# Kernel optimization log

Measured on AMD Instinct MI355X. Metric: run time of the kernel, lower is better.

The kernel has to match this reference:

```python
import jax, jax.numpy as jnp
import numpy as np

B, L, V, D = 512, 41, 4, 64        # batch, seq_len=41 (hard-coded in source), vocab=DNA, d_model=64
NL, DI, N, DTR, K = 3, 128, 16, 4, 4  # n_layer, d_inner=2*D, d_state, dt_rank=ceil(D/16), d_conv
NS = 3  # three parallel stacks (layers1/2/3)


def setup_inputs() -> dict:
    key = jax.random.key(0)
    ks = jax.random.split(key, 16)
    s = 0.02
    nrm = lambda k, sh: jax.random.normal(k, sh, jnp.float32) * s
    A_log = jnp.log(jnp.arange(1, N + 1, dtype=jnp.float32))  # S4D-real init
    return {
        "input_ids": jax.random.randint(ks[0], (B, L), 0, V),
        "embedding": nrm(ks[1], (V, D)),
        # per-stack, per-layer Mamba block params, stacked [NS, NL, ...]
        "in_proj": nrm(ks[2], (NS, NL, D, 2 * DI)),
        "conv_w": nrm(ks[3], (NS, NL, DI, 1, K)),
        "conv_b": jnp.zeros((NS, NL, DI), jnp.float32),
        "x_proj": nrm(ks[4], (NS, NL, DI, DTR + 2 * N)),
        "dt_w": nrm(ks[5], (NS, NL, DTR, DI)),
        "dt_b": jnp.full((NS, NL, DI), -2.0, jnp.float32),
        "A_log": jnp.broadcast_to(A_log, (NS, NL, DI, N)) + 0.0,
        "Dp": jnp.ones((NS, NL, DI), jnp.float32),
        "out_proj": nrm(ks[6], (NS, NL, DI, D)),
        "norm_w": jnp.ones((NS, NL, D), jnp.float32),
        "norm_f_w": jnp.ones((D,), jnp.float32),
        "fusion_w": jnp.zeros((NS,), jnp.float32),  # softmax-weighted fusion of the 3 representations
        # LastDense MLP head: 64*41 -> 384 -> 16 -> 1 (dropout is eval-mode identity)
        "W1": nrm(ks[7], (D * L, 384)), "b1": jnp.zeros((384,), jnp.float32),
        "W2": nrm(ks[8], (384, 16)), "b2": jnp.zeros((16,), jnp.float32),
        "W3": nrm(ks[9], (16, 1)), "b3": jnp.zeros((1,), jnp.float32),
    }


def rmsnorm(x, w, eps=1e-5):
    return x * jax.lax.rsqrt(jnp.mean(x * x, axis=-1, keepdims=True) + eps) * w


def silu(x):
    return x * jax.nn.sigmoid(x)


def mamba_block(x, ip, cw, cb, xp, dw, db, al, dp, op):
    # x: [B, L, D]
    bsz = x.shape[0]
    u, res = jnp.split(x @ ip, 2, axis=-1)  # each [B, L, DI]
    # causal depthwise conv1d (torch padding=3 then [..., :L] == left-pad K-1)
    uc = jax.lax.conv_general_dilated(
        u.transpose(0, 2, 1), cw, window_strides=(1,), padding=[(K - 1, 0)],
        feature_group_count=DI, dimension_numbers=("NCH", "OIH", "NCH"))
    u = silu((uc + cb[None, :, None]).transpose(0, 2, 1))  # [B, L, DI]
    dbl = u @ xp  # [B, L, DTR+2N]
    dt = jax.nn.softplus(dbl[..., :DTR] @ dw + db)           # [B, L, DI]
    Bm = dbl[..., DTR:DTR + N]                               # [B, L, N]
    C = dbl[..., DTR + N:]                                   # [B, L, N]
    A = -jnp.exp(al)                                         # [DI, N]
    dA = jnp.exp(dt[..., None] * A)                          # [B, L, DI, N]
    dBu = dt[..., None] * Bm[:, :, None, :] * u[..., None]   # [B, L, DI, N]

    def step(h, xs):
        dA_t, dBu_t, C_t = xs
        h = dA_t * h + dBu_t                                 # [B, DI, N]
        return h, jnp.einsum("bdn,bn->bd", h, C_t)

    h0 = jnp.zeros((bsz, DI, N), x.dtype)
    _, ys = jax.lax.scan(step, h0, (dA.transpose(1, 0, 2, 3), dBu.transpose(1, 0, 2, 3), C.transpose(1, 0, 2)))
    y = ys.transpose(1, 0, 2) + u * dp                       # [B, L, DI]
    return (y * silu(res)) @ op                              # [B, L, D]


def _forward(input_ids, embedding, in_proj, conv_w, conv_b, x_proj, dt_w, dt_b,
             A_log, Dp, out_proj, norm_w, norm_f_w, fusion_w, W1, b1, W2, b2, W3, b3):
    emb = embedding[input_ids]  # [B, L, D]

    def run_stack(ip, cw, cb, xp, dw, db, al, dp, op, nw):
        x = emb
        for i in range(NL):  # residual: x + MambaBlock(RMSNorm(x))
            x = x + mamba_block(rmsnorm(x, nw[i]), ip[i], cw[i], cb[i], xp[i], dw[i], db[i], al[i], dp[i], op[i])
        return x

    stack_out = jax.vmap(run_stack)(in_proj, conv_w, conv_b, x_proj, dt_w, dt_b,
                                    A_log, Dp, out_proj, norm_w)  # [NS, B, L, D]
    stack_out = rmsnorm(stack_out, norm_f_w)  # final norm_f per stack
    fused = jnp.einsum("s,sbld->bld", jax.nn.softmax(fusion_w), stack_out)  # fusion of 3 reps
    flat = fused.reshape(fused.shape[0], L * D)
    h = jax.nn.relu(flat @ W1 + b1)
    h = jax.nn.relu(h @ W2 + b2)
    logits = (h @ W3 + b3)[:, 0]
    return jax.nn.sigmoid(logits)  # [B]


def reference(input_ids, embedding, in_proj, conv_w, conv_b, x_proj, dt_w, dt_b,
              A_log, Dp, out_proj, norm_w, norm_f_w, fusion_w, W1, b1, W2, b2, W3, b3):
    return _forward(input_ids, embedding, in_proj, conv_w, conv_b, x_proj, dt_w, dt_b,
                    A_log, Dp, out_proj, norm_w, norm_f_w, fusion_w, W1, b1, W2, b2, W3, b3)
```

## Files before the change

### kernel.cpp

```cpp
#include <hip/hip_runtime.h>
#include <hip/hip_bf16.h>
#include <math.h>

#define Bq  512
#define Lq  41
#define Vq  4
#define Dq  64
#define NLq 3
#define DIq 128
#define Nq  16
#define DTRq 4
#define Kq  4
#define NSq 3
#define H1q 384
#define H2q 16
#define FLATq (Lq*Dq)

typedef __attribute__((ext_vector_type(8))) short frag8;
typedef __attribute__((ext_vector_type(4))) float f32x4;

__device__ __forceinline__ float b2f(unsigned short u) {
    union { float f; unsigned int i; } v; v.i = ((unsigned int)u) << 16; return v.f;
}
__device__ __forceinline__ unsigned short f2b_rne(float f) {
    union { float f; unsigned int i; } v; v.f = f;
    unsigned int x = v.i;
    return (unsigned short)((x + 0x7fffu + ((x >> 16) & 1u)) >> 16);
}
__device__ __forceinline__ unsigned short f2b_tr(float f) {
    union { float f; unsigned int i; } v; v.f = f;
    return (unsigned short)(v.i >> 16);
}
__device__ __forceinline__ float fast_rcp(float x) { return __builtin_amdgcn_rcpf(x); }

__global__ __launch_bounds__(256) void prep_kernel(const float* __restrict__ W1,
                                                   const float* __restrict__ in_proj,
                                                   const float* __restrict__ x_proj,
                                                   const float* __restrict__ out_proj,
                                                   unsigned short* __restrict__ W1b,
                                                   unsigned short* __restrict__ Wb_in,
                                                   unsigned short* __restrict__ xp_b,
                                                   unsigned short* __restrict__ op_b) {
    const int bx = blockIdx.x;
    if (bx < 246) {
        __shared__ float t[64][65];
        const int k0 = (bx / 6) * 64, n0 = (bx % 6) * 64;
        for (int idx = threadIdx.x; idx < 4096; idx += 256) {
            int kr = idx >> 6, nc = idx & 63;
            t[kr][nc] = W1[(size_t)(k0 + kr) * H1q + n0 + nc];
        }
        __syncthreads();
        for (int idx = threadIdx.x; idx < 4096; idx += 256) {
            int nr = idx >> 6, kc = idx & 63;
            W1b[(size_t)(n0 + nr) * FLATq + k0 + kc] = f2b_rne(t[kc][nr]);
        }
        return;
    }
    int idx = (bx - 246) * 256 + threadIdx.x;
    if (idx < 9*256*64) {
        int sl = idx >> 14, rem = idx & 16383;
        int n = rem >> 6, k = rem & 63;
        Wb_in[idx] = f2b_rne(in_proj[(size_t)sl*16384 + k*256 + n]);
    } else if (idx < 9*256*64 + 9*48*128) {
        int i2 = idx - 9*256*64;
        int sl = i2 / 6144, rem = i2 % 6144;
        int c = rem >> 7, k = rem & 127;
        float v = (c < 36) ? x_proj[(size_t)sl*(128*36) + k*36 + c] : 0.f;
        xp_b[i2] = f2b_rne(v);
    } else if (idx < 9*256*64 + 9*48*128 + 9*64*128) {
        int i3 = idx - (9*256*64 + 9*48*128);
        int sl = i3 >> 13, rem = i3 & 8191;
        int n = rem >> 7, k = rem & 127;
        op_b[i3] = f2b_rne(out_proj[(size_t)sl*8192 + k*64 + n]);
    }
}

__global__ __launch_bounds__(256, 4) void mamba_stack(
    unsigned short* __restrict__ Xn,
    const int* __restrict__ ids,
    const float* __restrict__ emb,
    const unsigned short* __restrict__ Wb_in,
    const float* __restrict__ conv_w,
    const float* __restrict__ conv_b,
    const unsigned short* __restrict__ xp_b,
    const float* __restrict__ dt_w,
    const float* __restrict__ dt_b,
    const float* __restrict__ A_log,
    const float* __restrict__ Dp,
    const unsigned short* __restrict__ op_b,
    const float* __restrict__ norm_w,
    const float* __restrict__ norm_f_w,
    const float* __restrict__ fusion_w)
{
    const int b = blockIdx.x, s = blockIdx.y, tid = threadIdx.x;
    const int wave = tid >> 6, lane = tid & 63;
    const int nl = lane & 15, quad = lane >> 4;

    __shared__ float          xt  [Lq][64];
    __shared__ unsigned short u_lb[48][136];
    __shared__ unsigned short rs_lb[Lq][128];
    __shared__ __align__(16) char un_buf[6912];
    unsigned short (*xn_lb)[72] = (unsigned short(*)[72])un_buf;
    float          (*dbl_s)[40] = (float(*)[40])un_buf;

    for (int l = wave; l < Lq; l += 4) {
        int id = ids[b * Lq + l];
        xt[l][lane] = emb[id * Dq + lane];
    }

    for (int layer = 0; layer < NLq; ++layer) {
        const int sl = s * NLq + layer;

        {
            const float nwv = norm_w[(size_t)sl * Dq + lane];
            for (int l = wave; l < 48; l += 4) {
                if (l < Lq) {
                    float v  = xt[l][lane];
                    float ss = v * v;
                    #pragma unroll
                    for (int off = 32; off; off >>= 1) ss += __shfl_xor(ss, off, 64);
                    float scale = __builtin_amdgcn_rsqf(ss * (1.0f / Dq) + 1e-5f);
                    xn_lb[l][lane] = f2b_tr(v * scale * nwv);
                } else {
                    xn_lb[l][lane] = 0;
                }
            }
        }
        __syncthreads();

        {
            #pragma unroll
            for (int t = 0; t < 12; ++t) {
                const int id = wave * 12 + t;
                const int mt = id >> 4, nt = id & 15;
                const unsigned short* Wp = Wb_in + ((size_t)(sl * 256 + nt * 16 + nl)) * 64 + quad * 8;
                frag8 a0 = *(const frag8*)&xn_lb[mt * 16 + nl][quad * 8];
                frag8 a1 = *(const frag8*)&xn_lb[mt * 16 + nl][32 + quad * 8];
                frag8 b0 = *(const frag8*)&Wp[0];
                frag8 b1 = *(const frag8*)&Wp[32];
                f32x4 c = {0.f, 0.f, 0.f, 0.f};
                c = __builtin_amdgcn_mfma_f32_16x16x32_bf16(a0, b0, c, 0, 0, 0);
                c = __builtin_amdgcn_mfma_f32_16x16x32_bf16(a1, b1, c, 0, 0, 0);
                const int col = nt * 16 + nl;
                const int r0 = mt * 16 + quad * 4;
                if (col < DIq) {
                    #pragma unroll
                    for (int r = 0; r < 4; ++r) u_lb[r0 + r][col] = f2b_tr(c[r]);
                } else {
                    const int d = col - DIq;
                    #pragma unroll
                    for (int r = 0; r < 4; ++r) {
                        int row = r0 + r;
                        if (row < Lq) {
                            float v = c[r];
                            rs_lb[row][d] = f2b_tr(v * fast_rcp(1.f + __expf(-v)));
                        }
                    }
                }
            }
        }
        __syncthreads();

        {
            const float* cw = conv_w + (size_t)sl * (DIq * Kq);
            const int d = tid >> 1, half = tid & 1;
            const float c0 = cw[d*4+0], c1 = cw[d*4+1], c2 = cw[d*4+2], c3 = cw[d*4+3];
            const float cbv = conv_b[(size_t)sl * DIq + d];
            float w0 = 0.f, w1 = 0.f, w2 = 0.f;
            if (half) { w0 = b2f(u_lb[18][d]); w1 = b2f(u_lb[19][d]); w2 = b2f(u_lb[20][d]); }
            const int base = half ? 21 : 0;
            const int cnt  = half ? 20 : 21;
            for (int i = 0; i < cnt; ++i) {
                int l = base + i;
                float cur = b2f(u_lb[l][d]);
                float a = fmaf(w0, c0, fmaf(w1, c1, fmaf(w2, c2, fmaf(cur, c3, cbv))));
                u_lb[l][d] = f2b_tr(a * fast_rcp(1.f + __expf(-a)));
                w0 = w1; w1 = w2; w2 = cur;
            }
        }
        __syncthreads();

        {
            for (int t = wave; t < 9; t += 4) {
                const int mt = t / 3, ct = t % 3;
                f32x4 c = {0.f, 0.f, 0.f, 0.f};
                #pragma unroll
                for (int kt = 0; kt < 4; ++kt) {
                    frag8 a  = *(const frag8*)&u_lb[mt * 16 + nl][kt * 32 + quad * 8];
                    frag8 bb = *(const frag8*)&xp_b[((size_t)(sl * 48 + ct * 16 + nl)) * 128 + kt * 32 + quad * 8];
                    c = __builtin_amdgcn_mfma_f32_16x16x32_bf16(a, bb, c, 0, 0, 0);
                }
                const int col = ct * 16 + nl, r0 = mt * 16 + quad * 4;
                if (col < 40) {
                    #pragma unroll
                    for (int r = 0; r < 4; ++r) {
                        int row = r0 + r;
                        if (row < Lq) dbl_s[row][col] = c[r];
                    }
                }
            }
        }
        __syncthreads();

        {
            const int d = tid >> 1, half = tid & 1;
            const float* al = A_log + (size_t)sl * (DIq * Nq) + d * Nq + half * 8;
            float A2[8], h[8];
            #pragma unroll
            for (int n = 0; n < 8; ++n) {
                A2[n] = -__expf(al[n]) * 1.442695041f;
                h[n] = 0.f;
            }
            const float* dw = dt_w + (size_t)sl * (DTRq * DIq);
            const float dw0 = dw[d], dw1 = dw[DIq + d], dw2 = dw[2*DIq + d], dw3 = dw[3*DIq + d];
            const float dbv = dt_b[(size_t)sl * DIq + d];
            const float dpd = Dp[(size_t)sl * DIq + d];
            for (int l = 0; l < Lq; ++l) {
                float4 q0 = *(const float4*)&dbl_s[l][0];
                float x  = fmaf(q0.x, dw0, fmaf(q0.y, dw1, fmaf(q0.z, dw2, fmaf(q0.w, dw3, dbv))));
                float dt_ = fmaxf(x, 0.f) + __logf(1.f + __expf(-fabsf(x)));
                float u_  = b2f(u_lb[l][d]);
                float rsv = b2f(rs_lb[l][d]);
                float4 B0 = *(const float4*)&dbl_s[l][4  + half * 8];
                float4 B1 = *(const float4*)&dbl_s[l][8  + half * 8];
                float4 C0 = *(const float4*)&dbl_s[l][20 + half * 8];
                float4 C1 = *(const float4*)&dbl_s[l][24 + half * 8];
                float dtu = dt_ * u_;
                float Bv[8] = {B0.x,B0.y,B0.z,B0.w,B1.x,B1.y,B1.z,B1.w};
                float Cv[8] = {C0.x,C0.y,C0.z,C0.w,C1.x,C1.y,C1.z,C1.w};
                float y = 0.f;
                #pragma unroll
                for (int n = 0; n < 8; ++n) {
                    float dA = __builtin_amdgcn_exp2f(dt_ * A2[n]);
                    h[n] = fmaf(dA, h[n], Bv[n] * dtu);
                    y    = fmaf(h[n], Cv[n], y);
                }
                y += __shfl_xor(y, 1, 64);
                if (!half) u_lb[l][d] = f2b_tr(fmaf(u_, dpd, y) * rsv);
            }
        }
        __syncthreads();

        {
            const int ntG = wave;
            for (int mt = 0; mt < 3; ++mt) {
                f32x4 c = {0.f, 0.f, 0.f, 0.f};
                #pragma unroll
                for (int kt = 0; kt < 4; ++kt) {
                    frag8 a  = *(const frag8*)&u_lb[mt * 16 + nl][kt * 32 + quad * 8];
                    frag8 bb = *(const frag8*)&op_b[((size_t)(sl * 64 + ntG * 16 + nl)) * 128 + kt * 32 + quad * 8];
                    c = __builtin_amdgcn_mfma_f32_16x16x32_bf16(a, bb, c, 0, 0, 0);
                }
                const int j = ntG * 16 + nl, r0 = mt * 16 + quad * 4;
                #pragma unroll
                for (int r = 0; r < 4; ++r) {
                    int row = r0 + r;
                    if (row < Lq) xt[row][j] += c[r];
                }
            }
        }
        __syncthreads();
    }

    {
        float fw0 = fusion_w[0], fw1 = fusion_w[1], fw2 = fusion_w[2];
        float mx = fmaxf(fw0, fmaxf(fw1, fw2));
        float e0 = __expf(fw0 - mx), e1 = __expf(fw1 - mx), e2 = __expf(fw2 - mx);
        float sw = (s == 0 ? e0 : (s == 1 ? e1 : e2)) * fast_rcp(e0 + e1 + e2);
        float nf = norm_f_w[lane] * sw;
        unsigned short* xr = Xn + ((size_t)s * Bq + b) * FLATq;
        for (int l = wave; l < Lq; l += 4) {
            float v  = xt[l][lane];
            float ss = v * v;
            #pragma unroll
            for (int off = 32; off; off >>= 1) ss += __shfl_xor(ss, off, 64);
            float scale = __builtin_amdgcn_rsqf(ss * (1.0f / Dq) + 1e-5f);
            xr[l * Dq + lane] = f2b_tr(v * scale * nf);
        }
    }
}

__global__ __launch_bounds__(256) void head_gemm1(const unsigned short* __restrict__ Xn,
                                                  const unsigned short* __restrict__ W1b,
                                                  const float* __restrict__ b1,
                                                  float* __restrict__ H1) {
    const int tid = threadIdx.x;
    const int wave = tid >> 6, lane = tid & 63;
    const int nl = lane & 15, quad = lane >> 4;
    const int mt = blockIdx.x, nt = blockIdx.y;

    __shared__ float red[4][16][17];

    const int kbeg = (wave < 2) ? wave * 21 : 42 + (wave - 2) * 20;
    const int kcnt = (wave < 2) ? 21 : 20;
    const size_t SB = (size_t)Bq * FLATq;
    const unsigned short* A0 = Xn  + (size_t)(mt * 16 + nl) * FLATq + quad * 8;
    const unsigned short* Br = W1b + (size_t)(nt * 16 + nl) * FLATq + quad * 8;

    f32x4 c = {0.f, 0.f, 0.f, 0.f};
    for (int ks = kbeg; ks < kbeg + kcnt; ++ks) {
        const int off = ks * 32;
        frag8 bb = *(const frag8*)(Br + off);
        frag8 a0 = *(const frag8*)(A0 + off);
        frag8 a1 = *(const frag8*)(A0 + SB + off);
        frag8 a2 = *(const frag8*)(A0 + 2 * SB + off);
        c = __builtin_amdgcn_mfma_f32_16x16x32_bf16(a0, bb, c, 0, 0, 0);
        c = __builtin_amdgcn_mfma_f32_16x16x32_bf16(a1, bb, c, 0, 0, 0);
        c = __builtin_amdgcn_mfma_f32_16x16x32_bf16(a2, bb, c, 0, 0, 0);
    }
    #pragma unroll
    for (int r = 0; r < 4; ++r) red[wave][quad * 4 + r][nl] = c[r];
    __syncthreads();

    const int row = tid >> 4, colv = tid & 15;
    float acc = red[0][row][colv] + red[1][row][colv]
              + red[2][row][colv] + red[3][row][colv];
    const int col = nt * 16 + colv;
    H1[(size_t)(mt * 16 + row) * H1q + col] = fmaxf(acc + b1[col], 0.f);
}

__global__ __launch_bounds__(256) void head_final(const float* __restrict__ H1,
                                                  const float* __restrict__ W2,
                                                  const float* __restrict__ b2,
                                                  const float* __restrict__ W3,
                                                  const float* __restrict__ b3,
                                                  float* __restrict__ out) {
    const int b0 = blockIdx.x * 16, tid = threadIdx.x;
    __shared__ float H1s[16 * H1q];
    __shared__ float h2s[16][16];
    for (int idx = tid; idx < 16 * H1q; idx += 256)
        H1s[idx] = H1[(size_t)b0 * H1q + idx];
    __syncthreads();
    {
        const int row = tid >> 4, g = tid & 15;
        float acc = b2[g];
        for (int k = 0; k < H1q; ++k)
            acc = fmaf(H1s[row * H1q + k], W2[k * H2q + g], acc);
        h2s[row][g] = fmaxf(acc, 0.f);
    }
    __syncthreads();
    if (tid < 16) {
        float z = b3[0];
        #pragma unroll
        for (int k = 0; k < H2q; ++k) z = fmaf(h2s[tid][k], W3[k], z);
        out[b0 + tid] = fast_rcp(1.f + __expf(-z));
    }
}

extern "C" void kernel_launch(void* const* d_in, const int* in_sizes, int n_in,
                              void* d_out, int out_size, void* d_ws, size_t ws_size,
                              hipStream_t stream) {
    const int*   ids      = (const int*)  d_in[0];
    const float* emb      = (const float*)d_in[1];
    const float* in_proj  = (const float*)d_in[2];
    const float* conv_w   = (const float*)d_in[3];
    const float* conv_b   = (const float*)d_in[4];
    const float* x_proj   = (const float*)d_in[5];
    const float* dt_w     = (const float*)d_in[6];
    const float* dt_b     = (const float*)d_in[7];
    const float* A_log    = (const float*)d_in[8];
    const float* Dp       = (const float*)d_in[9];
    const float* out_proj = (const float*)d_in[10];
    const float* norm_w   = (const float*)d_in[11];
    const float* norm_f_w = (const float*)d_in[12];
    const float* fusion_w = (const float*)d_in[13];
    const float* W1       = (const float*)d_in[14];
    const float* b1       = (const float*)d_in[15];
    const float* W2       = (const float*)d_in[16];
    const float* b2       = (const float*)d_in[17];
    const float* W3       = (const float*)d_in[18];
    const float* b3       = (const float*)d_in[19];
    float* out = (float*)d_out;

    unsigned short* Xn    = (unsigned short*)d_ws;
    unsigned short* Wb_in = Xn    + (size_t)NSq * Bq * FLATq;
    unsigned short* xp_b  = Wb_in + 9*256*64;
    unsigned short* op_b  = xp_b  + 9*48*128;
    unsigned short* W1b   = op_b  + 9*64*128;
    float*          H1    = (float*)(W1b + (size_t)H1q * FLATq);

    hipLaunchKernelGGL(prep_kernel, dim3(246 + 1080), dim3(256), 0, stream,
                       W1, in_proj, x_proj, out_proj, W1b, Wb_in, xp_b, op_b);

    hipLaunchKernelGGL(mamba_stack, dim3(Bq, NSq), dim3(256), 0, stream,
                       Xn, ids, emb, Wb_in, conv_w, conv_b, xp_b, dt_w, dt_b,
                       A_log, Dp, op_b, norm_w, norm_f_w, fusion_w);

    hipLaunchKernelGGL(head_gemm1, dim3(Bq/16, H1q/64), dim3(256), 0, stream,
                       Xn, W1b, b1, H1);

    hipLaunchKernelGGL(head_final, dim3(Bq/16), dim3(256), 0, stream,
                       H1, W2, b2, W3, b3, out);
}
```

Baseline: 310.9 us.

## Keep Mamba residual stream in registers, raise occupancy, reuse A tiles in head GEMM

The residual activations move from a shared-memory array into per-lane registers laid out to match the MFMA output fragment. RMSNorm therefore becomes a 16-lane shuffle reduction plus a small cross-wave scratch reduction, and the out-proj accumulation adds straight into registers. Shared-memory buffers are trimmed so occupancy can rise from 4 to 6 blocks per CU, and padded tail rows are clamped on reads. The head GEMM now gives each block two output tiles that share the same A fragments, halving the grid. Bf16 conversion switches from truncation to the library round-to-nearest routine, which costs a few extra ALU ops per conversion.

```diff
diff --git a/kernel.cpp b/kernel.cpp
--- a/kernel.cpp
+++ b/kernel.cpp
@@ -22,14 +22,9 @@
 __device__ __forceinline__ float b2f(unsigned short u) {
     union { float f; unsigned int i; } v; v.i = ((unsigned int)u) << 16; return v.f;
 }
-__device__ __forceinline__ unsigned short f2b_rne(float f) {
-    union { float f; unsigned int i; } v; v.f = f;
-    unsigned int x = v.i;
-    return (unsigned short)((x + 0x7fffu + ((x >> 16) & 1u)) >> 16);
-}
-__device__ __forceinline__ unsigned short f2b_tr(float f) {
-    union { float f; unsigned int i; } v; v.f = f;
-    return (unsigned short)(v.i >> 16);
+__device__ __forceinline__ unsigned short f2b(float f) {
+    __hip_bfloat16 h = __float2bfloat16(f);
+    return *reinterpret_cast<unsigned short*>(&h);
 }
 __device__ __forceinline__ float fast_rcp(float x) { return __builtin_amdgcn_rcpf(x); }
 
@@ -52,7 +47,7 @@
         __syncthreads();
         for (int idx = threadIdx.x; idx < 4096; idx += 256) {
             int nr = idx >> 6, kc = idx & 63;
-            W1b[(size_t)(n0 + nr) * FLATq + k0 + kc] = f2b_rne(t[kc][nr]);
+            W1b[(size_t)(n0 + nr) * FLATq + k0 + kc] = f2b(t[kc][nr]);
         }
         return;
     }
@@ -60,22 +55,22 @@
     if (idx < 9*256*64) {
         int sl = idx >> 14, rem = idx & 16383;
         int n = rem >> 6, k = rem & 63;
-        Wb_in[idx] = f2b_rne(in_proj[(size_t)sl*16384 + k*256 + n]);
+        Wb_in[idx] = f2b(in_proj[(size_t)sl*16384 + k*256 + n]);
     } else if (idx < 9*256*64 + 9*48*128) {
         int i2 = idx - 9*256*64;
         int sl = i2 / 6144, rem = i2 % 6144;
         int c = rem >> 7, k = rem & 127;
         float v = (c < 36) ? x_proj[(size_t)sl*(128*36) + k*36 + c] : 0.f;
-        xp_b[i2] = f2b_rne(v);
+        xp_b[i2] = f2b(v);
     } else if (idx < 9*256*64 + 9*48*128 + 9*64*128) {
         int i3 = idx - (9*256*64 + 9*48*128);
         int sl = i3 >> 13, rem = i3 & 8191;
         int n = rem >> 7, k = rem & 127;
-        op_b[i3] = f2b_rne(out_proj[(size_t)sl*8192 + k*64 + n]);
-    }
-}
-
-__global__ __launch_bounds__(256, 4) void mamba_stack(
+        op_b[i3] = f2b(out_proj[(size_t)sl*8192 + k*64 + n]);
+    }
+}
+
+__global__ __launch_bounds__(256, 6) void mamba_stack(
     unsigned short* __restrict__ Xn,
     const int* __restrict__ ids,
     const float* __restrict__ emb,
@@ -95,34 +90,56 @@
     const int b = blockIdx.x, s = blockIdx.y, tid = threadIdx.x;
     const int wave = tid >> 6, lane = tid & 63;
     const int nl = lane & 15, quad = lane >> 4;
-
-    __shared__ float          xt  [Lq][64];
-    __shared__ unsigned short u_lb[48][136];
+    const int col = wave * 16 + nl;
+
+    __shared__ unsigned short u_lb[Lq][128];
     __shared__ unsigned short rs_lb[Lq][128];
-    __shared__ __align__(16) char un_buf[6912];
+    __shared__ __align__(16) char un_buf[5904];
     unsigned short (*xn_lb)[72] = (unsigned short(*)[72])un_buf;
-    float          (*dbl_s)[40] = (float(*)[40])un_buf;
-
-    for (int l = wave; l < Lq; l += 4) {
-        int id = ids[b * Lq + l];
-        xt[l][lane] = emb[id * Dq + lane];
+    float          (*dbl_s)[36] = (float(*)[36])un_buf;
+    float* scratch = (float*)&rs_lb[0][0];
+
+    float xt[3][4];
+    #pragma unroll
+    for (int mt = 0; mt < 3; ++mt) {
+        #pragma unroll
+        for (int r = 0; r < 4; ++r) {
+            int row = mt * 16 + quad * 4 + r;
+            xt[mt][r] = (row < Lq) ? emb[ids[b * Lq + row] * Dq + col] : 0.f;
+        }
     }
 
     for (int layer = 0; layer < NLq; ++layer) {
         const int sl = s * NLq + layer;
 
         {
-            const float nwv = norm_w[(size_t)sl * Dq + lane];
-            for (int l = wave; l < 48; l += 4) {
-                if (l < Lq) {
-                    float v  = xt[l][lane];
+            const float nwv = norm_w[(size_t)sl * Dq + col];
+            #pragma unroll
+            for (int mt = 0; mt < 3; ++mt) {
+                #pragma unroll
+                for (int r = 0; r < 4; ++r) {
+                    float v = xt[mt][r];
                     float ss = v * v;
-                    #pragma unroll
-                    for (int off = 32; off; off >>= 1) ss += __shfl_xor(ss, off, 64);
-                    float scale = __builtin_amdgcn_rsqf(ss * (1.0f / Dq) + 1e-5f);
-                    xn_lb[l][lane] = f2b_tr(v * scale * nwv);
-                } else {
-                    xn_lb[l][lane] = 0;
+                    ss += __shfl_xor(ss, 1, 64);
+                    ss += __shfl_xor(ss, 2, 64);
+                    ss += __shfl_xor(ss, 4, 64);
+                    ss += __shfl_xor(ss, 8, 64);
+                    int row = mt * 16 + quad * 4 + r;
+                    if (nl == 0 && row < Lq) scratch[wave * 48 + row] = ss;
+                }
+            }
+            __syncthreads();
+            #pragma unroll
+            for (int mt = 0; mt < 3; ++mt) {
+                #pragma unroll
+                for (int r = 0; r < 4; ++r) {
+                    int row = mt * 16 + quad * 4 + r;
+                    if (row < Lq) {
+                        float ss = scratch[row] + scratch[48 + row]
+                                 + scratch[96 + row] + scratch[144 + row];
+                        float sc = __builtin_amdgcn_rsqf(ss * (1.0f / Dq) + 1e-5f);
+                        xn_lb[row][col] = f2b(xt[mt][r] * sc * nwv);
+                    }
                 }
             }
         }
@@ -133,27 +150,31 @@
             for (int t = 0; t < 12; ++t) {
                 const int id = wave * 12 + t;
                 const int mt = id >> 4, nt = id & 15;
+                const int ra = (mt == 2) ? min(32 + nl, Lq - 1) : (mt * 16 + nl);
                 const unsigned short* Wp = Wb_in + ((size_t)(sl * 256 + nt * 16 + nl)) * 64 + quad * 8;
-                frag8 a0 = *(const frag8*)&xn_lb[mt * 16 + nl][quad * 8];
-                frag8 a1 = *(const frag8*)&xn_lb[mt * 16 + nl][32 + quad * 8];
+                frag8 a0 = *(const frag8*)&xn_lb[ra][quad * 8];
+                frag8 a1 = *(const frag8*)&xn_lb[ra][32 + quad * 8];
                 frag8 b0 = *(const frag8*)&Wp[0];
                 frag8 b1 = *(const frag8*)&Wp[32];
                 f32x4 c = {0.f, 0.f, 0.f, 0.f};
                 c = __builtin_amdgcn_mfma_f32_16x16x32_bf16(a0, b0, c, 0, 0, 0);
                 c = __builtin_amdgcn_mfma_f32_16x16x32_bf16(a1, b1, c, 0, 0, 0);
-                const int col = nt * 16 + nl;
+                const int cc = nt * 16 + nl;
                 const int r0 = mt * 16 + quad * 4;
-                if (col < DIq) {
+                if (cc < DIq) {
                     #pragma unroll
-                    for (int r = 0; r < 4; ++r) u_lb[r0 + r][col] = f2b_tr(c[r]);
+                    for (int r = 0; r < 4; ++r) {
+                        int row = r0 + r;
+                        if (mt < 2 || row < Lq) u_lb[row][cc] = f2b(c[r]);
+                    }
                 } else {
-                    const int d = col - DIq;
+                    const int d = cc - DIq;
                     #pragma unroll
                     for (int r = 0; r < 4; ++r) {
                         int row = r0 + r;
                         if (row < Lq) {
                             float v = c[r];
-                            rs_lb[row][d] = f2b_tr(v * fast_rcp(1.f + __expf(-v)));
+                            rs_lb[row][d] = f2b(v * fast_rcp(1.f + __expf(-v)));
                         }
                     }
                 }
@@ -174,7 +195,7 @@
                 int l = base + i;
                 float cur = b2f(u_lb[l][d]);
                 float a = fmaf(w0, c0, fmaf(w1, c1, fmaf(w2, c2, fmaf(cur, c3, cbv))));
-                u_lb[l][d] = f2b_tr(a * fast_rcp(1.f + __expf(-a)));
+                u_lb[l][d] = f2b(a * fast_rcp(1.f + __expf(-a)));
                 w0 = w1; w1 = w2; w2 = cur;
             }
         }
@@ -183,19 +204,20 @@
         {
             for (int t = wave; t < 9; t += 4) {
                 const int mt = t / 3, ct = t % 3;
+                const int ra = (mt == 2) ? min(32 + nl, Lq - 1) : (mt * 16 + nl);
                 f32x4 c = {0.f, 0.f, 0.f, 0.f};
                 #pragma unroll
                 for (int kt = 0; kt < 4; ++kt) {
-                    frag8 a  = *(const frag8*)&u_lb[mt * 16 + nl][kt * 32 + quad * 8];
+                    frag8 a  = *(const frag8*)&u_lb[ra][kt * 32 + quad * 8];
                     frag8 bb = *(const frag8*)&xp_b[((size_t)(sl * 48 + ct * 16 + nl)) * 128 + kt * 32 + quad * 8];
                     c = __builtin_amdgcn_mfma_f32_16x16x32_bf16(a, bb, c, 0, 0, 0);
                 }
-                const int col = ct * 16 + nl, r0 = mt * 16 + quad * 4;
-                if (col < 40) {
+                const int cc = ct * 16 + nl, r0 = mt * 16 + quad * 4;
+                if (cc < 36) {
                     #pragma unroll
                     for (int r = 0; r < 4; ++r) {
                         int row = r0 + r;
-                        if (row < Lq) dbl_s[row][col] = c[r];
+                        if (row < Lq) dbl_s[row][cc] = c[r];
                     }
                 }
             }
@@ -236,27 +258,24 @@
                     y    = fmaf(h[n], Cv[n], y);
                 }
                 y += __shfl_xor(y, 1, 64);
-                if (!half) u_lb[l][d] = f2b_tr(fmaf(u_, dpd, y) * rsv);
-            }
-        }
-        __syncthreads();
-
-        {
-            const int ntG = wave;
+                if (!half) u_lb[l][d] = f2b(fmaf(u_, dpd, y) * rsv);
+            }
+        }
+        __syncthreads();
+
+        {
+            #pragma unroll
             for (int mt = 0; mt < 3; ++mt) {
+                const int ra = (mt == 2) ? min(32 + nl, Lq - 1) : (mt * 16 + nl);
                 f32x4 c = {0.f, 0.f, 0.f, 0.f};
                 #pragma unroll
                 for (int kt = 0; kt < 4; ++kt) {
-                    frag8 a  = *(const frag8*)&u_lb[mt * 16 + nl][kt * 32 + quad * 8];
-                    frag8 bb = *(const frag8*)&op_b[((size_t)(sl * 64 + ntG * 16 + nl)) * 128 + kt * 32 + quad * 8];
+                    frag8 a  = *(const frag8*)&u_lb[ra][kt * 32 + quad * 8];
+                    frag8 bb = *(const frag8*)&op_b[((size_t)(sl * 64 + wave * 16 + nl)) * 128 + kt * 32 + quad * 8];
                     c = __builtin_amdgcn_mfma_f32_16x16x32_bf16(a, bb, c, 0, 0, 0);
                 }
-                const int j = ntG * 16 + nl, r0 = mt * 16 + quad * 4;
-                #pragma unroll
-                for (int r = 0; r < 4; ++r) {
-                    int row = r0 + r;
-                    if (row < Lq) xt[row][j] += c[r];
-                }
+                #pragma unroll
+                for (int r = 0; r < 4; ++r) xt[mt][r] += c[r];
             }
         }
         __syncthreads();
@@ -267,15 +286,35 @@
         float mx = fmaxf(fw0, fmaxf(fw1, fw2));
         float e0 = __expf(fw0 - mx), e1 = __expf(fw1 - mx), e2 = __expf(fw2 - mx);
         float sw = (s == 0 ? e0 : (s == 1 ? e1 : e2)) * fast_rcp(e0 + e1 + e2);
-        float nf = norm_f_w[lane] * sw;
+        float nf = norm_f_w[col] * sw;
         unsigned short* xr = Xn + ((size_t)s * Bq + b) * FLATq;
-        for (int l = wave; l < Lq; l += 4) {
-            float v  = xt[l][lane];
-            float ss = v * v;
-            #pragma unroll
-            for (int off = 32; off; off >>= 1) ss += __shfl_xor(ss, off, 64);
-            float scale = __builtin_amdgcn_rsqf(ss * (1.0f / Dq) + 1e-5f);
-            xr[l * Dq + lane] = f2b_tr(v * scale * nf);
+        #pragma unroll
+        for (int mt = 0; mt < 3; ++mt) {
+            #pragma unroll
+            for (int r = 0; r < 4; ++r) {
+                float v = xt[mt][r];
+                float ss = v * v;
+                ss += __shfl_xor(ss, 1, 64);
+                ss += __shfl_xor(ss, 2, 64);
+                ss += __shfl_xor(ss, 4, 64);
+                ss += __shfl_xor(ss, 8, 64);
+                int row = mt * 16 + quad * 4 + r;
+                if (nl == 0 && row < Lq) scratch[wave * 48 + row] = ss;
+            }
+        }
+        __syncthreads();
+        #pragma unroll
+        for (int mt = 0; mt < 3; ++mt) {
+            #pragma unroll
+            for (int r = 0; r < 4; ++r) {
+                int row = mt * 16 + quad * 4 + r;
+                if (row < Lq) {
+                    float ss = scratch[row] + scratch[48 + row]
+                             + scratch[96 + row] + scratch[144 + row];
+                    float sc = __builtin_amdgcn_rsqf(ss * (1.0f / Dq) + 1e-5f);
+                    xr[row * Dq + col] = f2b(xt[mt][r] * sc * nf);
+                }
+            }
         }
     }
 }
@@ -287,36 +326,47 @@
     const int tid = threadIdx.x;
     const int wave = tid >> 6, lane = tid & 63;
     const int nl = lane & 15, quad = lane >> 4;
-    const int mt = blockIdx.x, nt = blockIdx.y;
-
-    __shared__ float red[4][16][17];
+    const int mt = blockIdx.x, np = blockIdx.y;
+
+    __shared__ float red[2][4][16][17];
 
     const int kbeg = (wave < 2) ? wave * 21 : 42 + (wave - 2) * 20;
     const int kcnt = (wave < 2) ? 21 : 20;
     const size_t SB = (size_t)Bq * FLATq;
     const unsigned short* A0 = Xn  + (size_t)(mt * 16 + nl) * FLATq + quad * 8;
-    const unsigned short* Br = W1b + (size_t)(nt * 16 + nl) * FLATq + quad * 8;
-
-    f32x4 c = {0.f, 0.f, 0.f, 0.f};
+    const unsigned short* Bp0 = W1b + (size_t)((np    ) * 16 + nl) * FLATq + quad * 8;
+    const unsigned short* Bp1 = W1b + (size_t)((np + 3) * 16 + nl) * FLATq + quad * 8;
+
+    f32x4 c0 = {0.f,0.f,0.f,0.f}, c1 = {0.f,0.f,0.f,0.f};
     for (int ks = kbeg; ks < kbeg + kcnt; ++ks) {
         const int off = ks * 32;
-        frag8 bb = *(const frag8*)(Br + off);
         frag8 a0 = *(const frag8*)(A0 + off);
         frag8 a1 = *(const frag8*)(A0 + SB + off);
         frag8 a2 = *(const frag8*)(A0 + 2 * SB + off);
-        c = __builtin_amdgcn_mfma_f32_16x16x32_bf16(a0, bb, c, 0, 0, 0);
-        c = __builtin_amdgcn_mfma_f32_16x16x32_bf16(a1, bb, c, 0, 0, 0);
-        c = __builtin_amdgcn_mfma_f32_16x16x32_bf16(a2, bb, c, 0, 0, 0);
+        frag8 w0 = *(const frag8*)(Bp0 + off);
+        frag8 w1 = *(const frag8*)(Bp1 + off);
+        c0 = __builtin_amdgcn_mfma_f32_16x16x32_bf16(a0, w0, c0, 0, 0, 0);
+        c1 = __builtin_amdgcn_mfma_f32_16x16x32_bf16(a0, w1, c1, 0, 0, 0);
+        c0 = __builtin_amdgcn_mfma_f32_16x16x32_bf16(a1, w0, c0, 0, 0, 0);
+        c1 = __builtin_amdgcn_mfma_f32_16x16x32_bf16(a1, w1, c1, 0, 0, 0);
+        c0 = __builtin_amdgcn_mfma_f32_16x16x32_bf16(a2, w0, c0, 0, 0, 0);
+        c1 = __builtin_amdgcn_mfma_f32_16x16x32_bf16(a2, w1, c1, 0, 0, 0);
     }
     #pragma unroll
-    for (int r = 0; r < 4; ++r) red[wave][quad * 4 + r][nl] = c[r];
+    for (int r = 0; r < 4; ++r) {
+        red[0][wave][quad * 4 + r][nl] = c0[r];
+        red[1][wave][quad * 4 + r][nl] = c1[r];
+    }
     __syncthreads();
 
-    const int row = tid >> 4, colv = tid & 15;
-    float acc = red[0][row][colv] + red[1][row][colv]
-              + red[2][row][colv] + red[3][row][colv];
-    const int col = nt * 16 + colv;
-    H1[(size_t)(mt * 16 + row) * H1q + col] = fmaxf(acc + b1[col], 0.f);
+    const int row = (tid >> 4) & 15, colv = tid & 15;
+    #pragma unroll
+    for (int t = 0; t < 2; ++t) {
+        float acc = red[t][0][row][colv] + red[t][1][row][colv]
+                  + red[t][2][row][colv] + red[t][3][row][colv];
+        const int colg = (np + 3 * t) * 16 + colv;
+        H1[(size_t)(mt * 16 + row) * H1q + colg] = fmaxf(acc + b1[colg], 0.f);
+    }
 }
 
 __global__ __launch_bounds__(256) void head_final(const float* __restrict__ H1,
@@ -386,7 +436,7 @@
                        Xn, ids, emb, Wb_in, conv_w, conv_b, xp_b, dt_w, dt_b,
                        A_log, Dp, op_b, norm_w, norm_f_w, fusion_w);
 
-    hipLaunchKernelGGL(head_gemm1, dim3(Bq/16, H1q/64), dim3(256), 0, stream,
+    hipLaunchKernelGGL(head_gemm1, dim3(Bq/16, 3), dim3(256), 0, stream,
                        Xn, W1b, b1, H1);
 
     hipLaunchKernelGGL(head_final, dim3(Bq/16), dim3(256), 0, stream,
```

After: 376.5 us. 21.1% more time.

## Fuse stack outputs via fp32 atomics and retile head GEMM with LDS staging

Applied to the files above, without the earlier changes.

Each stack's final normalized output is now atomically added into a single fp32 flat buffer, replacing three separate bf16 copies, so the head GEMM reads one fused input instead of three. The head GEMM is rewritten as a 64x64-tiled kernel that stages swizzled bf16 A and W tiles in shared memory, replacing the split-K per-wave reduction. The manual bf16 conversions are also replaced with the library round-to-nearest conversion everywhere. This adds a memset and atomic contention across the three stacks, and the head grid drops to 48 blocks, which may underfill the device.

```diff
diff --git a/kernel.cpp b/kernel.cpp
--- a/kernel.cpp
+++ b/kernel.cpp
@@ -22,14 +22,9 @@
 __device__ __forceinline__ float b2f(unsigned short u) {
     union { float f; unsigned int i; } v; v.i = ((unsigned int)u) << 16; return v.f;
 }
-__device__ __forceinline__ unsigned short f2b_rne(float f) {
-    union { float f; unsigned int i; } v; v.f = f;
-    unsigned int x = v.i;
-    return (unsigned short)((x + 0x7fffu + ((x >> 16) & 1u)) >> 16);
-}
-__device__ __forceinline__ unsigned short f2b_tr(float f) {
-    union { float f; unsigned int i; } v; v.f = f;
-    return (unsigned short)(v.i >> 16);
+__device__ __forceinline__ unsigned short f2b(float f) {
+    __hip_bfloat16 h = __float2bfloat16(f);
+    return *reinterpret_cast<unsigned short*>(&h);
 }
 __device__ __forceinline__ float fast_rcp(float x) { return __builtin_amdgcn_rcpf(x); }
 
@@ -52,7 +47,7 @@
         __syncthreads();
         for (int idx = threadIdx.x; idx < 4096; idx += 256) {
             int nr = idx >> 6, kc = idx & 63;
-            W1b[(size_t)(n0 + nr) * FLATq + k0 + kc] = f2b_rne(t[kc][nr]);
+            W1b[(size_t)(n0 + nr) * FLATq + k0 + kc] = f2b(t[kc][nr]);
         }
         return;
     }
@@ -60,23 +55,23 @@
     if (idx < 9*256*64) {
         int sl = idx >> 14, rem = idx & 16383;
         int n = rem >> 6, k = rem & 63;
-        Wb_in[idx] = f2b_rne(in_proj[(size_t)sl*16384 + k*256 + n]);
+        Wb_in[idx] = f2b(in_proj[(size_t)sl*16384 + k*256 + n]);
     } else if (idx < 9*256*64 + 9*48*128) {
         int i2 = idx - 9*256*64;
         int sl = i2 / 6144, rem = i2 % 6144;
         int c = rem >> 7, k = rem & 127;
         float v = (c < 36) ? x_proj[(size_t)sl*(128*36) + k*36 + c] : 0.f;
-        xp_b[i2] = f2b_rne(v);
+        xp_b[i2] = f2b(v);
     } else if (idx < 9*256*64 + 9*48*128 + 9*64*128) {
         int i3 = idx - (9*256*64 + 9*48*128);
         int sl = i3 >> 13, rem = i3 & 8191;
         int n = rem >> 7, k = rem & 127;
-        op_b[i3] = f2b_rne(out_proj[(size_t)sl*8192 + k*64 + n]);
+        op_b[i3] = f2b(out_proj[(size_t)sl*8192 + k*64 + n]);
     }
 }
 
 __global__ __launch_bounds__(256, 4) void mamba_stack(
-    unsigned short* __restrict__ Xn,
+    float* __restrict__ Flat_f,
     const int* __restrict__ ids,
     const float* __restrict__ emb,
     const unsigned short* __restrict__ Wb_in,
@@ -119,8 +114,8 @@
                     float ss = v * v;
                     #pragma unroll
                     for (int off = 32; off; off >>= 1) ss += __shfl_xor(ss, off, 64);
-                    float scale = __builtin_amdgcn_rsqf(ss * (1.0f / Dq) + 1e-5f);
-                    xn_lb[l][lane] = f2b_tr(v * scale * nwv);
+                    float sc = __builtin_amdgcn_rsqf(ss * (1.0f / Dq) + 1e-5f);
+                    xn_lb[l][lane] = f2b(v * sc * nwv);
                 } else {
                     xn_lb[l][lane] = 0;
                 }
@@ -141,19 +136,19 @@
                 f32x4 c = {0.f, 0.f, 0.f, 0.f};
                 c = __builtin_amdgcn_mfma_f32_16x16x32_bf16(a0, b0, c, 0, 0, 0);
                 c = __builtin_amdgcn_mfma_f32_16x16x32_bf16(a1, b1, c, 0, 0, 0);
-                const int col = nt * 16 + nl;
+                const int cc = nt * 16 + nl;
                 const int r0 = mt * 16 + quad * 4;
-                if (col < DIq) {
+                if (cc < DIq) {
                     #pragma unroll
-                    for (int r = 0; r < 4; ++r) u_lb[r0 + r][col] = f2b_tr(c[r]);
+                    for (int r = 0; r < 4; ++r) u_lb[r0 + r][cc] = f2b(c[r]);
                 } else {
-                    const int d = col - DIq;
+                    const int d = cc - DIq;
                     #pragma unroll
                     for (int r = 0; r < 4; ++r) {
                         int row = r0 + r;
                         if (row < Lq) {
                             float v = c[r];
-                            rs_lb[row][d] = f2b_tr(v * fast_rcp(1.f + __expf(-v)));
+                            rs_lb[row][d] = f2b(v * fast_rcp(1.f + __expf(-v)));
                         }
                     }
                 }
@@ -174,7 +169,7 @@
                 int l = base + i;
                 float cur = b2f(u_lb[l][d]);
                 float a = fmaf(w0, c0, fmaf(w1, c1, fmaf(w2, c2, fmaf(cur, c3, cbv))));
-                u_lb[l][d] = f2b_tr(a * fast_rcp(1.f + __expf(-a)));
+                u_lb[l][d] = f2b(a * fast_rcp(1.f + __expf(-a)));
                 w0 = w1; w1 = w2; w2 = cur;
             }
         }
@@ -190,12 +185,12 @@
                     frag8 bb = *(const frag8*)&xp_b[((size_t)(sl * 48 + ct * 16 + nl)) * 128 + kt * 32 + quad * 8];
                     c = __builtin_amdgcn_mfma_f32_16x16x32_bf16(a, bb, c, 0, 0, 0);
                 }
-                const int col = ct * 16 + nl, r0 = mt * 16 + quad * 4;
-                if (col < 40) {
+                const int cc = ct * 16 + nl, r0 = mt * 16 + quad * 4;
+                if (cc < 40) {
                     #pragma unroll
                     for (int r = 0; r < 4; ++r) {
                         int row = r0 + r;
-                        if (row < Lq) dbl_s[row][col] = c[r];
+                        if (row < Lq) dbl_s[row][cc] = c[r];
                     }
                 }
             }
@@ -236,22 +231,22 @@
                     y    = fmaf(h[n], Cv[n], y);
                 }
                 y += __shfl_xor(y, 1, 64);
-                if (!half) u_lb[l][d] = f2b_tr(fmaf(u_, dpd, y) * rsv);
-            }
-        }
-        __syncthreads();
-
-        {
-            const int ntG = wave;
+                if (!half) u_lb[l][d] = f2b(fmaf(u_, dpd, y) * rsv);
+            }
+        }
+        __syncthreads();
+
+        {
+            #pragma unroll
             for (int mt = 0; mt < 3; ++mt) {
                 f32x4 c = {0.f, 0.f, 0.f, 0.f};
                 #pragma unroll
                 for (int kt = 0; kt < 4; ++kt) {
                     frag8 a  = *(const frag8*)&u_lb[mt * 16 + nl][kt * 32 + quad * 8];
-                    frag8 bb = *(const frag8*)&op_b[((size_t)(sl * 64 + ntG * 16 + nl)) * 128 + kt * 32 + quad * 8];
+                    frag8 bb = *(const frag8*)&op_b[((size_t)(sl * 64 + wave * 16 + nl)) * 128 + kt * 32 + quad * 8];
                     c = __builtin_amdgcn_mfma_f32_16x16x32_bf16(a, bb, c, 0, 0, 0);
                 }
-                const int j = ntG * 16 + nl, r0 = mt * 16 + quad * 4;
+                const int j = wave * 16 + nl, r0 = mt * 16 + quad * 4;
                 #pragma unroll
                 for (int r = 0; r < 4; ++r) {
                     int row = r0 + r;
@@ -268,55 +263,79 @@
         float e0 = __expf(fw0 - mx), e1 = __expf(fw1 - mx), e2 = __expf(fw2 - mx);
         float sw = (s == 0 ? e0 : (s == 1 ? e1 : e2)) * fast_rcp(e0 + e1 + e2);
         float nf = norm_f_w[lane] * sw;
-        unsigned short* xr = Xn + ((size_t)s * Bq + b) * FLATq;
+        float* fr = Flat_f + (size_t)b * FLATq;
         for (int l = wave; l < Lq; l += 4) {
             float v  = xt[l][lane];
             float ss = v * v;
             #pragma unroll
             for (int off = 32; off; off >>= 1) ss += __shfl_xor(ss, off, 64);
-            float scale = __builtin_amdgcn_rsqf(ss * (1.0f / Dq) + 1e-5f);
-            xr[l * Dq + lane] = f2b_tr(v * scale * nf);
-        }
-    }
-}
-
-__global__ __launch_bounds__(256) void head_gemm1(const unsigned short* __restrict__ Xn,
-                                                  const unsigned short* __restrict__ W1b,
-                                                  const float* __restrict__ b1,
-                                                  float* __restrict__ H1) {
+            float sc = __builtin_amdgcn_rsqf(ss * (1.0f / Dq) + 1e-5f);
+            atomicAdd(&fr[l * Dq + lane], v * sc * nf);
+        }
+    }
+}
+
+__global__ __launch_bounds__(256) void head_gemm(const float* __restrict__ Flat_f,
+                                                 const unsigned short* __restrict__ W1b,
+                                                 const float* __restrict__ b1,
+                                                 float* __restrict__ H1) {
     const int tid = threadIdx.x;
     const int wave = tid >> 6, lane = tid & 63;
     const int nl = lane & 15, quad = lane >> 4;
-    const int mt = blockIdx.x, nt = blockIdx.y;
-
-    __shared__ float red[4][16][17];
-
-    const int kbeg = (wave < 2) ? wave * 21 : 42 + (wave - 2) * 20;
-    const int kcnt = (wave < 2) ? 21 : 20;
-    const size_t SB = (size_t)Bq * FLATq;
-    const unsigned short* A0 = Xn  + (size_t)(mt * 16 + nl) * FLATq + quad * 8;
-    const unsigned short* Br = W1b + (size_t)(nt * 16 + nl) * FLATq + quad * 8;
-
-    f32x4 c = {0.f, 0.f, 0.f, 0.f};
-    for (int ks = kbeg; ks < kbeg + kcnt; ++ks) {
-        const int off = ks * 32;
-        frag8 bb = *(const frag8*)(Br + off);
-        frag8 a0 = *(const frag8*)(A0 + off);
-        frag8 a1 = *(const frag8*)(A0 + SB + off);
-        frag8 a2 = *(const frag8*)(A0 + 2 * SB + off);
-        c = __builtin_amdgcn_mfma_f32_16x16x32_bf16(a0, bb, c, 0, 0, 0);
-        c = __builtin_amdgcn_mfma_f32_16x16x32_bf16(a1, bb, c, 0, 0, 0);
-        c = __builtin_amdgcn_mfma_f32_16x16x32_bf16(a2, bb, c, 0, 0, 0);
-    }
+    const int r0 = blockIdx.x * 64, n0 = blockIdx.y * 64;
+
+    __shared__ unsigned short As[64 * 64];
+    __shared__ unsigned short Ws[64 * 64];
+
+    f32x4 acc[4] = {{0,0,0,0},{0,0,0,0},{0,0,0,0},{0,0,0,0}};
+
+    for (int kk = 0; kk < 41; ++kk) {
+        const int k0 = kk * 64;
+        __syncthreads();
+        #pragma unroll
+        for (int u0 = 0; u0 < 512; u0 += 256) {
+            const int u = u0 + tid;
+            const int row = u >> 3, g = u & 7;
+            const float* src = Flat_f + (size_t)(r0 + row) * FLATq + k0 + g * 8;
+            float4 f0 = *(const float4*)src;
+            float4 f1 = *(const float4*)(src + 4);
+            union { frag8 v; unsigned short us[8]; } pk;
+            pk.us[0] = f2b(f0.x); pk.us[1] = f2b(f0.y);
+            pk.us[2] = f2b(f0.z); pk.us[3] = f2b(f0.w);
+            pk.us[4] = f2b(f1.x); pk.us[5] = f2b(f1.y);
+            pk.us[6] = f2b(f1.z); pk.us[7] = f2b(f1.w);
+            *(frag8*)&As[row * 64 + ((g + row) & 7) * 8] = pk.v;
+        }
+        #pragma unroll
+        for (int u0 = 0; u0 < 512; u0 += 256) {
+            const int u = u0 + tid;
+            const int row = u >> 3, g = u & 7;
+            frag8 w = *(const frag8*)(W1b + (size_t)(n0 + row) * FLATq + k0 + g * 8);
+            *(frag8*)&Ws[row * 64 + ((g + row) & 7) * 8] = w;
+        }
+        __syncthreads();
+        #pragma unroll
+        for (int ks = 0; ks < 2; ++ks) {
+            const int arow = wave * 16 + nl;
+            frag8 a = *(const frag8*)&As[arow * 64 + (((ks * 4 + quad) + arow) & 7) * 8];
+            #pragma unroll
+            for (int ct = 0; ct < 4; ++ct) {
+                const int brow = ct * 16 + nl;
+                frag8 bb = *(const frag8*)&Ws[brow * 64 + (((ks * 4 + quad) + brow) & 7) * 8];
+                acc[ct] = __builtin_amdgcn_mfma_f32_16x16x32_bf16(a, bb, acc[ct], 0, 0, 0);
+            }
+        }
+    }
+
     #pragma unroll
-    for (int r = 0; r < 4; ++r) red[wave][quad * 4 + r][nl] = c[r];
-    __syncthreads();
-
-    const int row = tid >> 4, colv = tid & 15;
-    float acc = red[0][row][colv] + red[1][row][colv]
-              + red[2][row][colv] + red[3][row][colv];
-    const int col = nt * 16 + colv;
-    H1[(size_t)(mt * 16 + row) * H1q + col] = fmaxf(acc + b1[col], 0.f);
+    for (int ct = 0; ct < 4; ++ct) {
+        #pragma unroll
+        for (int r = 0; r < 4; ++r) {
+            const int row = r0 + wave * 16 + quad * 4 + r;
+            const int col = n0 + ct * 16 + nl;
+            H1[(size_t)row * H1q + col] = fmaxf(acc[ct][r] + b1[col], 0.f);
+        }
+    }
 }
 
 __global__ __launch_bounds__(256) void head_final(const float* __restrict__ H1,
@@ -372,22 +391,24 @@
     const float* b3       = (const float*)d_in[19];
     float* out = (float*)d_out;
 
-    unsigned short* Xn    = (unsigned short*)d_ws;
-    unsigned short* Wb_in = Xn    + (size_t)NSq * Bq * FLATq;
-    unsigned short* xp_b  = Wb_in + 9*256*64;
-    unsigned short* op_b  = xp_b  + 9*48*128;
-    unsigned short* W1b   = op_b  + 9*64*128;
-    float*          H1    = (float*)(W1b + (size_t)H1q * FLATq);
+    float*          Flat_f = (float*)d_ws;
+    unsigned short* Wb_in  = (unsigned short*)(Flat_f + (size_t)Bq * FLATq);
+    unsigned short* xp_b   = Wb_in + 9*256*64;
+    unsigned short* op_b   = xp_b  + 9*48*128;
+    unsigned short* W1b    = op_b  + 9*64*128;
+    float*          H1     = (float*)(W1b + (size_t)H1q * FLATq);
 
     hipLaunchKernelGGL(prep_kernel, dim3(246 + 1080), dim3(256), 0, stream,
                        W1, in_proj, x_proj, out_proj, W1b, Wb_in, xp_b, op_b);
 
+    hipMemsetAsync(Flat_f, 0, (size_t)Bq * FLATq * sizeof(float), stream);
+
     hipLaunchKernelGGL(mamba_stack, dim3(Bq, NSq), dim3(256), 0, stream,
-                       Xn, ids, emb, Wb_in, conv_w, conv_b, xp_b, dt_w, dt_b,
+                       Flat_f, ids, emb, Wb_in, conv_w, conv_b, xp_b, dt_w, dt_b,
                        A_log, Dp, op_b, norm_w, norm_f_w, fusion_w);
 
-    hipLaunchKernelGGL(head_gemm1, dim3(Bq/16, H1q/64), dim3(256), 0, stream,
-                       Xn, W1b, b1, H1);
+    hipLaunchKernelGGL(head_gemm, dim3(8, 6), dim3(256), 0, stream,
+                       Flat_f, W1b, b1, H1);
 
     hipLaunchKernelGGL(head_final, dim3(Bq/16), dim3(256), 0, stream,
                        H1, W2, b2, W3, b3, out);
```

New measurement: 371.5 us. 1.2x slower.
